# Kernel optimization log

Hardware: AMD Instinct MI355X
Metric: run time of the kernel (lower is better)

Reference implementation:

```python
import jax, jax.numpy as jnp
import numpy as np
from jax import lax

WINDOW_SIZE = 11
SIGMA = 1.5
MAX_VAL = 1.0
C1 = (0.01 * MAX_VAL) ** 2
C2 = (0.03 * MAX_VAL) ** 2
PAD = (WINDOW_SIZE - 1) // 2


def _gaussian_kernel2d(ksize: int, sigma: float) -> jnp.ndarray:
    x = jnp.arange(ksize, dtype=jnp.float32) - ksize // 2
    g = jnp.exp(-(x ** 2) / (2.0 * sigma ** 2))
    g = g / jnp.sum(g)
    return jnp.outer(g, g)  # [k, k]


def _filter2d(x: jnp.ndarray, kernel2d: jnp.ndarray) -> jnp.ndarray:
    # depthwise conv: x [B,C,H,W], kernel repeated per channel -> [C,1,k,k]
    c = x.shape[1]
    k = jnp.broadcast_to(kernel2d[None, None], (c, 1, WINDOW_SIZE, WINDOW_SIZE)).astype(x.dtype)
    return lax.conv_general_dilated(
        x, k,
        window_strides=(1, 1),
        padding=((PAD, PAD), (PAD, PAD)),
        dimension_numbers=("NCHW", "OIHW", "NCHW"),
        feature_group_count=c,
    )


def setup_inputs() -> dict:
    key = jax.random.key(0)
    k1, k2 = jax.random.split(key)
    img1 = jax.random.uniform(k1, (16, 3, 512, 512), dtype=jnp.float32)
    img2 = jax.random.uniform(k2, (16, 3, 512, 512), dtype=jnp.float32)
    return {"img1": img1, "img2": img2}


def reference(img1, img2):
    kernel = _gaussian_kernel2d(WINDOW_SIZE, SIGMA)
    mu1 = _filter2d(img1, kernel)
    mu2 = _filter2d(img2, kernel)
    mu1_sq = mu1 * mu1
    mu2_sq = mu2 * mu2
    mu1_mu2 = mu1 * mu2
    sigma1_sq = _filter2d(img1 * img1, kernel) - mu1_sq
    sigma2_sq = _filter2d(img2 * img2, kernel) - mu2_sq
    sigma12 = _filter2d(img1 * img2, kernel) - mu1_mu2
    ssim_map = ((2.0 * mu1_mu2 + C1) * (2.0 * sigma12 + C2)) / (
        (mu1_sq + mu2_sq + C1) * (sigma1_sq + sigma2_sq + C2)
    )
    loss = jnp.clip(1.0 - ssim_map, 0.0, 1.0) / 2.0
    return jnp.mean(loss)  # reduction='mean'
```

## Files before the change

kernel.cpp:

```cpp
#include <hip/hip_runtime.h>


#define BATCH  16
#define CHAN   3
#define H_     512
#define W_     512
#define HW     (H_ * W_)
#define CH_H   64
#define NPIX   ((long)BATCH*CHAN*H_*W_)

#define GW0 0.0010284f
#define GW1 0.0075988f
#define GW2 0.0360008f
#define GW3 0.1093554f
#define GW4 0.2130056f
#define GW5 0.2660117f

typedef float v2 __attribute__((ext_vector_type(2)));

__device__ __forceinline__ float wg(int k) {
    return (k == 0 || k == 10) ? GW0
         : (k == 1 || k == 9)  ? GW1
         : (k == 2 || k == 8)  ? GW2
         : (k == 3 || k == 7)  ? GW3
         : (k == 4 || k == 6)  ? GW4 : GW5;
}

__device__ __forceinline__ v2 pfma(v2 a, v2 b, v2 c) {
#if __has_builtin(__builtin_elementwise_fma)
    return __builtin_elementwise_fma(a, b, c);
#else
    v2 r; r.x = fmaf(a.x, b.x, c.x); r.y = fmaf(a.y, b.y, c.y); return r;
#endif
}
__device__ __forceinline__ v2 psfma(float s, v2 b, v2 c) {
    v2 sv; sv.x = s; sv.y = s;
    return pfma(sv, b, c);
}

__device__ __forceinline__ float ssim_retire(float mu1, float mu2,
                                             float x11, float x22, float x12) {
    const float c1 = 1.0e-4f;
    const float c2 = 9.0e-4f;
    float mu1s = mu1 * mu1;
    float mu2s = mu2 * mu2;
    float m12  = mu1 * mu2;
    float num  = (2.0f * m12 + c1) * (2.0f * (x12 - m12) + c2);
    float den  = (mu1s + mu2s + c1) * ((x11 - mu1s) + (x22 - mu2s) + c2);
    float l = 1.0f - num / den;
    return fminf(fmaxf(l, 0.0f), 1.0f);
}

#define DECL(i) v2 P##i = {0.f, 0.f}, Q##i = {0.f, 0.f}; float E##i = 0.f
#define ACCI(i) do { const float wj_ = wg(10 - (i));             \
    P##i = psfma(wj_, hmm, P##i);                                \
    Q##i = psfma(wj_, hss, Q##i);                                \
    E##i = fmaf(wj_, hm12, E##i); } while (0)
#define SHIFT(i, j) P##i = P##j; Q##i = Q##j; E##i = E##j

__global__ __launch_bounds__(256, 3) void ssim_kernel(const float* __restrict__ img1,
                                                      const float* __restrict__ img2,
                                                      float* __restrict__ out) {
    __shared__ __align__(16) v2 sp[4][80];
    __shared__ float wsum[4];

    const int tid  = threadIdx.x;
    const int lane = tid & 63;
    const int wv   = tid >> 6;

    const int wid   = blockIdx.x * 4 + wv;
    const int plane = wid >> 6;
    const int rem   = wid & 63;
    const int strip = rem & 7;
    const int chunk = rem >> 3;
    const int y0 = chunk * CH_H;
    const int c0 = strip * 64;

    const int  colg  = c0 - 5 + lane;
    const bool colOk = (colg >= 0);
    const int  colC  = colOk ? colg : 0;
    const int  colg2  = c0 + 59 + lane;
    const bool colOk2 = (lane < 11) && (colg2 < W_);
    const int  col2C  = colOk2 ? colg2 : 0;

    const size_t pb = (size_t)plane * HW;
    const float* __restrict__ p1  = img1 + pb + colC;
    const float* __restrict__ p2  = img2 + pb + colC;
    const float* __restrict__ p1b = img1 + pb + col2C;
    const float* __restrict__ p2b = img2 + pb + col2C;

    v2* st = sp[wv];

    DECL(0); DECL(1); DECL(2); DECL(3); DECL(4); DECL(5);
    DECL(6); DECL(7); DECL(8); DECL(9); DECL(10);
    float lsum = 0.0f;

    float cv1, cv2, cv1b, cv2b;
    {
        int r = y0 - 5;
        bool rok = (unsigned)r < (unsigned)H_;
        size_t off = (size_t)(rok ? r : 0) * W_;
        cv1  = (rok && colOk)  ? p1[off]  : 0.0f;
        cv2  = (rok && colOk)  ? p2[off]  : 0.0f;
        cv1b = (rok && colOk2) ? p1b[off] : 0.0f;
        cv2b = (rok && colOk2) ? p2b[off] : 0.0f;
    }

#pragma unroll 2
    for (int step = 0; step < 74; ++step) {
        const int yy = step - 10;

        {
            v2 v; v.x = cv1; v.y = cv2;
            st[lane] = v;
            if (lane < 11) { v2 vb; vb.x = cv1b; vb.y = cv2b; st[64 + lane] = vb; }
        }
        __asm__ __volatile__("" ::: "memory");

        {
            int r = y0 + yy + 6;
            bool rok = (unsigned)r < (unsigned)H_;
            size_t off = (size_t)(rok ? r : 0) * W_;
            cv1  = (rok && colOk)  ? p1[off]  : 0.0f;
            cv2  = (rok && colOk)  ? p2[off]  : 0.0f;
            cv1b = (rok && colOk2) ? p1b[off] : 0.0f;
            cv2b = (rok && colOk2) ? p2b[off] : 0.0f;
        }

        v2 hmm = {0.f, 0.f}, hss = {0.f, 0.f};
        float hm12 = 0.f;
#pragma unroll
        for (int k = 0; k < 11; ++k) {
            v2 ab = st[lane + k];
            float wk = wg(k);
            v2 t = ab;
            t.x *= wk; t.y *= wk;
            hmm += t;
            hss = pfma(t, ab, hss);
            hm12 = fmaf(t.x, ab.y, hm12);
        }
        __asm__ __volatile__("" ::: "memory");

        ACCI(0); ACCI(1); ACCI(2); ACCI(3); ACCI(4); ACCI(5);
        ACCI(6); ACCI(7); ACCI(8); ACCI(9); ACCI(10);

        if (yy >= 0) lsum += ssim_retire(P0.x, P0.y, Q0.x, Q0.y, E0);

        SHIFT(0, 1); SHIFT(1, 2); SHIFT(2, 3); SHIFT(3, 4); SHIFT(4, 5);
        SHIFT(5, 6); SHIFT(6, 7); SHIFT(7, 8); SHIFT(8, 9); SHIFT(9, 10);
        P10 = (v2){0.f, 0.f}; Q10 = (v2){0.f, 0.f}; E10 = 0.f;
    }

#pragma unroll
    for (int off = 32; off > 0; off >>= 1) lsum += __shfl_down(lsum, off);
    if (lane == 0) wsum[wv] = lsum;
    __syncthreads();
    if (tid == 0) {
        float bs = wsum[0] + wsum[1] + wsum[2] + wsum[3];
        atomicAdd(out, bs * (0.5f / (float)NPIX));
    }
}

extern "C" void kernel_launch(void* const* d_in, const int* in_sizes, int n_in,
                              void* d_out, int out_size, void* d_ws, size_t ws_size,
                              hipStream_t stream) {
    const float* img1 = (const float*)d_in[0];
    const float* img2 = (const float*)d_in[1];
    float* out = (float*)d_out;

    hipMemsetAsync(out, 0, sizeof(float), stream);

    ssim_kernel<<<dim3(8 * 8 * BATCH * CHAN / 4), 256, 0, stream>>>(img1, img2, out);
}
```

Measured before the change: 155.4 us.

## Halve row chunks, vectorize row loads, double-buffer LDS rows, use fast reciprocal

Result: slower. 213.1 us (+37.2%).

```diff
diff --git a/kernel.cpp b/kernel.cpp
--- a/kernel.cpp
+++ b/kernel.cpp
@@ -6,7 +6,8 @@
 #define H_     512
 #define W_     512
 #define HW     (H_ * W_)
-#define CH_H   64
+#define CH_H   32
+#define NSTEP  (CH_H + 10)
 #define NPIX   ((long)BATCH*CHAN*H_*W_)
 
 #define GW0 0.0010284f
@@ -16,7 +17,8 @@
 #define GW4 0.2130056f
 #define GW5 0.2660117f
 
-typedef float v2 __attribute__((ext_vector_type(2)));
+typedef float v2  __attribute__((ext_vector_type(2)));
+typedef float v4f __attribute__((ext_vector_type(4)));
 
 __device__ __forceinline__ float wg(int k) {
     return (k == 0 || k == 10) ? GW0
@@ -47,7 +49,11 @@
     float m12  = mu1 * mu2;
     float num  = (2.0f * m12 + c1) * (2.0f * (x12 - m12) + c2);
     float den  = (mu1s + mu2s + c1) * ((x11 - mu1s) + (x22 - mu2s) + c2);
+#if __has_builtin(__builtin_amdgcn_rcpf)
+    float l = 1.0f - num * __builtin_amdgcn_rcpf(den);
+#else
     float l = 1.0f - num / den;
+#endif
     return fminf(fmaxf(l, 0.0f), 1.0f);
 }
 
@@ -58,10 +64,10 @@
     E##i = fmaf(wj_, hm12, E##i); } while (0)
 #define SHIFT(i, j) P##i = P##j; Q##i = Q##j; E##i = E##j
 
-__global__ __launch_bounds__(256, 3) void ssim_kernel(const float* __restrict__ img1,
+__global__ __launch_bounds__(256, 6) void ssim_kernel(const float* __restrict__ img1,
                                                       const float* __restrict__ img2,
                                                       float* __restrict__ out) {
-    __shared__ __align__(16) v2 sp[4][80];
+    __shared__ __align__(16) v2 sp[4][2][80];
     __shared__ float wsum[4];
 
     const int tid  = threadIdx.x;
@@ -69,86 +75,85 @@
     const int wv   = tid >> 6;
 
     const int wid   = blockIdx.x * 4 + wv;
-    const int plane = wid >> 6;
-    const int rem   = wid & 63;
+    const int plane = wid >> 7;
+    const int rem   = wid & 127;
     const int strip = rem & 7;
     const int chunk = rem >> 3;
     const int y0 = chunk * CH_H;
     const int c0 = strip * 64;
 
-    const int  colg  = c0 - 5 + lane;
-    const bool colOk = (colg >= 0);
-    const int  colC  = colOk ? colg : 0;
-    const int  colg2  = c0 + 59 + lane;
-    const bool colOk2 = (lane < 11) && (colg2 < W_);
-    const int  col2C  = colOk2 ? colg2 : 0;
+    const int  cg   = c0 - 6 + 2 * lane;
+    const bool cok  = (cg >= 0) && (cg < W_) && (lane < 38);
+    const int  cix  = cok ? cg : 0;
+    const float msk = cok ? 1.0f : 0.0f;
 
     const size_t pb = (size_t)plane * HW;
-    const float* __restrict__ p1  = img1 + pb + colC;
-    const float* __restrict__ p2  = img2 + pb + colC;
-    const float* __restrict__ p1b = img1 + pb + col2C;
-    const float* __restrict__ p2b = img2 + pb + col2C;
+    const float* __restrict__ p1 = img1 + pb;
+    const float* __restrict__ p2 = img2 + pb;
 
-    v2* st = sp[wv];
+    v2 (*st)[80] = sp[wv];
 
     DECL(0); DECL(1); DECL(2); DECL(3); DECL(4); DECL(5);
     DECL(6); DECL(7); DECL(8); DECL(9); DECL(10);
     float lsum = 0.0f;
 
-    float cv1, cv2, cv1b, cv2b;
+    v2 cva = {0.f, 0.f}, cvb = {0.f, 0.f};
     {
         int r = y0 - 5;
-        bool rok = (unsigned)r < (unsigned)H_;
-        size_t off = (size_t)(rok ? r : 0) * W_;
-        cv1  = (rok && colOk)  ? p1[off]  : 0.0f;
-        cv2  = (rok && colOk)  ? p2[off]  : 0.0f;
-        cv1b = (rok && colOk2) ? p1b[off] : 0.0f;
-        cv2b = (rok && colOk2) ? p2b[off] : 0.0f;
+        if ((unsigned)r < (unsigned)H_) {
+            size_t off = (size_t)r * W_ + cix;
+            v2 a = *(const v2*)(p1 + off);
+            v2 b = *(const v2*)(p2 + off);
+            cva = a * msk; cvb = b * msk;
+        }
     }
 
-#pragma unroll 2
-    for (int step = 0; step < 74; ++step) {
-        const int yy = step - 10;
+#pragma unroll 1
+    for (int sb = 0; sb < NSTEP / 6; ++sb) {
+#pragma unroll
+        for (int j = 0; j < 6; ++j) {
+            const int step = sb * 6 + j;
+            const int par  = j & 1;
 
-        {
-            v2 v; v.x = cv1; v.y = cv2;
-            st[lane] = v;
-            if (lane < 11) { v2 vb; vb.x = cv1b; vb.y = cv2b; st[64 + lane] = vb; }
+            if (lane < 38) {
+                v4f w; w.x = cva.x; w.y = cvb.x; w.z = cva.y; w.w = cvb.y;
+                *(v4f*)&st[par][2 * lane] = w;
+            }
+            __asm__ __volatile__("" ::: "memory");
+
+            {
+                int r = y0 + step - 4;
+                cva = (v2){0.f, 0.f}; cvb = (v2){0.f, 0.f};
+                if ((unsigned)r < (unsigned)H_) {
+                    size_t off = (size_t)r * W_ + cix;
+                    v2 a = *(const v2*)(p1 + off);
+                    v2 b = *(const v2*)(p2 + off);
+                    cva = a * msk; cvb = b * msk;
+                }
+            }
+
+            v2 hmm = {0.f, 0.f}, hss = {0.f, 0.f};
+            float hm12 = 0.f;
+#pragma unroll
+            for (int k = 0; k < 11; ++k) {
+                v2 ab = st[par][lane + 1 + k];
+                float wk = wg(k);
+                v2 t = ab;
+                t.x *= wk; t.y *= wk;
+                hmm += t;
+                hss = pfma(t, ab, hss);
+                hm12 = fmaf(t.x, ab.y, hm12);
+            }
+
+            ACCI(0); ACCI(1); ACCI(2); ACCI(3); ACCI(4); ACCI(5);
+            ACCI(6); ACCI(7); ACCI(8); ACCI(9); ACCI(10);
+
+            if (step >= 10) lsum += ssim_retire(P0.x, P0.y, Q0.x, Q0.y, E0);
+
+            SHIFT(0, 1); SHIFT(1, 2); SHIFT(2, 3); SHIFT(3, 4); SHIFT(4, 5);
+            SHIFT(5, 6); SHIFT(6, 7); SHIFT(7, 8); SHIFT(8, 9); SHIFT(9, 10);
+            P10 = (v2){0.f, 0.f}; Q10 = (v2){0.f, 0.f}; E10 = 0.f;
         }
-        __asm__ __volatile__("" ::: "memory");
-
-        {
-            int r = y0 + yy + 6;
-            bool rok = (unsigned)r < (unsigned)H_;
-            size_t off = (size_t)(rok ? r : 0) * W_;
-            cv1  = (rok && colOk)  ? p1[off]  : 0.0f;
-            cv2  = (rok && colOk)  ? p2[off]  : 0.0f;
-            cv1b = (rok && colOk2) ? p1b[off] : 0.0f;
-            cv2b = (rok && colOk2) ? p2b[off] : 0.0f;
-        }
-
-        v2 hmm = {0.f, 0.f}, hss = {0.f, 0.f};
-        float hm12 = 0.f;
-#pragma unroll
-        for (int k = 0; k < 11; ++k) {
-            v2 ab = st[lane + k];
-            float wk = wg(k);
-            v2 t = ab;
-            t.x *= wk; t.y *= wk;
-            hmm += t;
-            hss = pfma(t, ab, hss);
-            hm12 = fmaf(t.x, ab.y, hm12);
-        }
-        __asm__ __volatile__("" ::: "memory");
-
-        ACCI(0); ACCI(1); ACCI(2); ACCI(3); ACCI(4); ACCI(5);
-        ACCI(6); ACCI(7); ACCI(8); ACCI(9); ACCI(10);
-
-        if (yy >= 0) lsum += ssim_retire(P0.x, P0.y, Q0.x, Q0.y, E0);
-
-        SHIFT(0, 1); SHIFT(1, 2); SHIFT(2, 3); SHIFT(3, 4); SHIFT(4, 5);
-        SHIFT(5, 6); SHIFT(6, 7); SHIFT(7, 8); SHIFT(8, 9); SHIFT(9, 10);
-        P10 = (v2){0.f, 0.f}; Q10 = (v2){0.f, 0.f}; E10 = 0.f;
     }
 
 #pragma unroll
@@ -170,5 +175,5 @@
 
     hipMemsetAsync(out, 0, sizeof(float), stream);
 
-    ssim_kernel<<<dim3(8 * 8 * BATCH * CHAN / 4), 256, 0, stream>>>(img1, img2, out);
+    ssim_kernel<<<dim3(8 * 16 * BATCH * CHAN / 4), 256, 0, stream>>>(img1, img2, out);
 }
```
